# Optimization experiments

Measured on AMD Instinct MI355X. Metric: run time of the kernel, lower is better.

## Reference

```python
import jax, jax.numpy as jnp
import numpy as np

N_FILLERS = 10000
N_ROLES = 256
FILLER_DIM = 256
ROLE_DIM = 256
HIDDEN = 1024
B, S = 64, 128


def setup_inputs() -> dict:
    key = jax.random.key(0)
    k1, k2, k3, k4, k5, k6 = jax.random.split(key, 6)
    roles = jax.random.randint(k1, (B, S), 0, N_ROLES, dtype=jnp.int64 if jax.config.jax_enable_x64 else jnp.int32)
    hidden = jax.random.normal(k2, (1, B, HIDDEN), dtype=jnp.float32)
    filler_emb = jax.random.normal(k3, (N_FILLERS, FILLER_DIM), dtype=jnp.float32)
    role_emb = jax.random.normal(k4, (N_ROLES, ROLE_DIM), dtype=jnp.float32)
    role_emb = role_emb.at[0].set(0.0)  # padding_idx=0
    W = jax.random.normal(k5, (FILLER_DIM * ROLE_DIM, HIDDEN), dtype=jnp.float32) / np.sqrt(HIDDEN)
    b = jax.random.normal(k6, (FILLER_DIM * ROLE_DIM,), dtype=jnp.float32) * 0.01
    return {"roles": roles, "hidden": hidden, "filler_emb": filler_emb, "role_emb": role_emb, "W": W, "b": b}


def reference(roles, hidden, filler_emb, role_emb, W, b):
    fd = filler_emb.shape[1]
    rd = role_emb.shape[1]
    # input_layer: (1, B, hidden) -> (1, B, fd*rd)
    h = hidden @ W.T + b
    # transpose(0,1).transpose(1,2).view(-1, fd, rd): (B, fd, rd)
    h = jnp.transpose(h, (1, 2, 0)).reshape(-1, fd, rd)
    # role embedding with padding_idx=0 (row 0 is zero)
    role_table = role_emb.at[0].set(0.0)
    roles_e = role_table[roles]  # (B, S, rd)
    # bmm(roles_emb, hidden^T): (B, S, rd) x (B, rd, fd) -> (B, S, fd)
    fg = jnp.einsum('bsr,bfr->bsf', roles_e, h)
    # L2 distance to filler codebook via squared-norm trick: (B, S, n_fillers)
    d2 = (jnp.sum(fg * fg, axis=-1, keepdims=True)
          - 2.0 * jnp.einsum('bsf,nf->bsn', fg, filler_emb)
          + jnp.sum(filler_emb * filler_emb, axis=-1))
    dists = jnp.sqrt(jnp.maximum(d2, 0.0))
    log_probs = jax.nn.log_softmax(-dists, axis=-1)  # (B, S, n_fillers)
    preds = jnp.argmax(log_probs, axis=-1)  # top-1 indices, (B, S)
    return log_probs, preds
```

## Files before the change

### kernel.cpp

```cpp
#include <hip/hip_runtime.h>
#include <hip/hip_bf16.h>
#include <float.h>
#include <math.h>

#define ROWS 8192
#define NF   10000
#define NPAD 10240

typedef short s8v __attribute__((ext_vector_type(8)));
typedef float f4v __attribute__((ext_vector_type(4)));

#define GLD16(g, l) __builtin_amdgcn_global_load_lds((const __attribute__((address_space(1))) void*)(g), (__attribute__((address_space(3))) void*)(l), 16, 0, 0)

__device__ inline unsigned short f2bf(float x) {
  __hip_bfloat16 h = __float2bfloat16(x);
  return __builtin_bit_cast(unsigned short, h);
}
__device__ inline float bf2f(unsigned short u) {
  __hip_bfloat16 h = __builtin_bit_cast(__hip_bfloat16, u);
  return __bfloat162float(h);
}

__global__ __launch_bounds__(256) void k_cvt_filler(const float* __restrict__ filler,
                                                    unsigned short* __restrict__ fl2,
                                                    float* __restrict__ fln) {
  int row = blockIdx.x * 4 + (threadIdx.x >> 6);
  int lane = threadIdx.x & 63;
  if (row >= NPAD) return;
  if (row < NF) {
    float4 v = reinterpret_cast<const float4*>(filler + (size_t)row * 256)[lane];
    float s = v.x * v.x + v.y * v.y + v.z * v.z + v.w * v.w;
    #pragma unroll
    for (int off = 32; off >= 1; off >>= 1) s += __shfl_xor(s, off, 64);
    if (lane == 0) fln[row] = s;
    float xs[4] = {v.x, v.y, v.z, v.w};
    unsigned short h[4], lo[4];
    #pragma unroll
    for (int j = 0; j < 4; ++j) { h[j] = f2bf(xs[j]); lo[j] = f2bf(xs[j] - bf2f(h[j])); }
    uint2 hh = make_uint2(h[0] | ((unsigned)h[1] << 16), h[2] | ((unsigned)h[3] << 16));
    uint2 ll = make_uint2(lo[0] | ((unsigned)lo[1] << 16), lo[2] | ((unsigned)lo[3] << 16));
    *reinterpret_cast<uint2*>(fl2 + (size_t)row * 512 + lane * 4) = hh;
    *reinterpret_cast<uint2*>(fl2 + (size_t)row * 512 + 256 + lane * 4) = ll;
  } else {
    *reinterpret_cast<uint2*>(fl2 + (size_t)row * 512 + lane * 4) = make_uint2(0, 0);
    *reinterpret_cast<uint2*>(fl2 + (size_t)row * 512 + 256 + lane * 4) = make_uint2(0, 0);
    if (lane == 0) fln[row] = 1e30f;
  }
}

__global__ __launch_bounds__(256) void k_gemm1(const float* __restrict__ hidden,
                                               const float* __restrict__ W,
                                               const float* __restrict__ bias,
                                               float* __restrict__ ht) {
  __shared__ float As[64][68];
  __shared__ float Bs[64][136];
  __shared__ float biasS[128];
  const int tid = threadIdx.x;
  const int nbase = blockIdx.x * 128;
  const int r = nbase >> 8;
  const int f0 = nbase & 255;
  const int tm = tid >> 4, tn = tid & 15;
  const int m0 = tm * 4, n0 = tn * 8;

  if (tid < 128) biasS[tid] = bias[(size_t)(f0 + tid) * 256 + r];

  float acc[4][8];
  #pragma unroll
  for (int i = 0; i < 4; ++i)
    #pragma unroll
    for (int j = 0; j < 8; ++j) acc[i][j] = 0.f;

  for (int kt = 0; kt < 16; ++kt) {
    __syncthreads();
    #pragma unroll
    for (int i = 0; i < 4; ++i) {
      int q = tid + i * 256;
      int b = q >> 4, kq = q & 15;
      float4 v = *reinterpret_cast<const float4*>(hidden + (size_t)b * 1024 + kt * 64 + kq * 4);
      As[kq * 4 + 0][b] = v.x;
      As[kq * 4 + 1][b] = v.y;
      As[kq * 4 + 2][b] = v.z;
      As[kq * 4 + 3][b] = v.w;
    }
    #pragma unroll
    for (int i = 0; i < 8; ++i) {
      int q = tid + i * 256;
      int nl = q >> 4, kq = q & 15;
      size_t wrow = (size_t)(f0 + nl) * 256 + r;
      float4 v = *reinterpret_cast<const float4*>(W + wrow * 1024 + kt * 64 + kq * 4);
      Bs[kq * 4 + 0][nl] = v.x;
      Bs[kq * 4 + 1][nl] = v.y;
      Bs[kq * 4 + 2][nl] = v.z;
      Bs[kq * 4 + 3][nl] = v.w;
    }
    __syncthreads();
    #pragma unroll
    for (int kk = 0; kk < 64; ++kk) {
      float4 a  = *reinterpret_cast<const float4*>(&As[kk][m0]);
      float4 b0 = *reinterpret_cast<const float4*>(&Bs[kk][n0]);
      float4 b1 = *reinterpret_cast<const float4*>(&Bs[kk][n0 + 4]);
      float av[4] = {a.x, a.y, a.z, a.w};
      float bv[8] = {b0.x, b0.y, b0.z, b0.w, b1.x, b1.y, b1.z, b1.w};
      #pragma unroll
      for (int i = 0; i < 4; ++i)
        #pragma unroll
        for (int j = 0; j < 8; ++j) acc[i][j] += av[i] * bv[j];
    }
  }
  #pragma unroll
  for (int i = 0; i < 4; ++i) {
    int b = m0 + i;
    float4 o0 = make_float4(acc[i][0] + biasS[n0 + 0], acc[i][1] + biasS[n0 + 1],
                            acc[i][2] + biasS[n0 + 2], acc[i][3] + biasS[n0 + 3]);
    float4 o1 = make_float4(acc[i][4] + biasS[n0 + 4], acc[i][5] + biasS[n0 + 5],
                            acc[i][6] + biasS[n0 + 6], acc[i][7] + biasS[n0 + 7]);
    float* p = ht + (size_t)b * 65536 + nbase + n0;
    *reinterpret_cast<float4*>(p)     = o0;
    *reinterpret_cast<float4*>(p + 4) = o1;
  }
}

__global__ __launch_bounds__(256) void k_fg2(const int* __restrict__ roles,
                                             const float* __restrict__ role_emb,
                                             const float* __restrict__ ht,
                                             unsigned short* __restrict__ fg2,
                                             float* __restrict__ fgn) {
  __shared__ float As[64][40];
  __shared__ float Bs[64][264];
  __shared__ int sidx[32];
  const int tid = threadIdx.x;
  const int b = blockIdx.x >> 2;
  const int sbase = (blockIdx.x & 3) * 32;
  const int tm = tid >> 5, tn = tid & 31;
  const int m0 = tm * 4, n0 = tn * 8;
  if (tid < 32) sidx[tid] = roles[b * 128 + sbase + tid];

  float acc[4][8];
  #pragma unroll
  for (int i = 0; i < 4; ++i)
    #pragma unroll
    for (int j = 0; j < 8; ++j) acc[i][j] = 0.f;

  for (int kt = 0; kt < 4; ++kt) {
    __syncthreads();
    #pragma unroll
    for (int i = 0; i < 2; ++i) {
      int q = tid + i * 256;
      int s = q >> 4, rq = q & 15;
      float4 v = *reinterpret_cast<const float4*>(role_emb + (size_t)sidx[s] * 256 + kt * 64 + rq * 4);
      As[rq * 4 + 0][s] = v.x;
      As[rq * 4 + 1][s] = v.y;
      As[rq * 4 + 2][s] = v.z;
      As[rq * 4 + 3][s] = v.w;
    }
    #pragma unroll
    for (int i = 0; i < 16; ++i) {
      int q = tid + i * 256;
      int rr = q >> 6, fq = q & 63;
      float4 v = *reinterpret_cast<const float4*>(ht + (size_t)b * 65536 + (size_t)(kt * 64 + rr) * 256 + fq * 4);
      *reinterpret_cast<float4*>(&Bs[rr][fq * 4]) = v;
    }
    __syncthreads();
    #pragma unroll
    for (int kk = 0; kk < 64; ++kk) {
      float4 a  = *reinterpret_cast<const float4*>(&As[kk][m0]);
      float4 b0 = *reinterpret_cast<const float4*>(&Bs[kk][n0]);
      float4 b1 = *reinterpret_cast<const float4*>(&Bs[kk][n0 + 4]);
      float av[4] = {a.x, a.y, a.z, a.w};
      float bv[8] = {b0.x, b0.y, b0.z, b0.w, b1.x, b1.y, b1.z, b1.w};
      #pragma unroll
      for (int i = 0; i < 4; ++i)
        #pragma unroll
        for (int j = 0; j < 8; ++j) acc[i][j] += av[i] * bv[j];
    }
  }
  #pragma unroll
  for (int i = 0; i < 4; ++i) {
    const int grow = b * 128 + sbase + m0 + i;
    float nrm = 0.f;
    unsigned int hp[4], lp[4];
    #pragma unroll
    for (int j = 0; j < 8; j += 2) {
      float x0 = acc[i][j], x1 = acc[i][j + 1];
      nrm += x0 * x0 + x1 * x1;
      unsigned short h0 = f2bf(x0), h1 = f2bf(x1);
      unsigned short l0 = f2bf(x0 - bf2f(h0)), l1 = f2bf(x1 - bf2f(h1));
      hp[j >> 1] = h0 | ((unsigned)h1 << 16);
      lp[j >> 1] = l0 | ((unsigned)l1 << 16);
    }
    *reinterpret_cast<uint4*>(fg2 + (size_t)grow * 512 + n0)       = make_uint4(hp[0], hp[1], hp[2], hp[3]);
    *reinterpret_cast<uint4*>(fg2 + (size_t)grow * 512 + 256 + n0) = make_uint4(lp[0], lp[1], lp[2], lp[3]);
    #pragma unroll
    for (int msk = 1; msk <= 16; msk <<= 1) nrm += __shfl_xor(nrm, msk, 64);
    if (tn == 0) fgn[grow] = nrm;
  }
}

__global__ __launch_bounds__(512, 4) void k_dist(const unsigned short* __restrict__ fg2,
                                                 const unsigned short* __restrict__ fl2,
                                                 const float* __restrict__ fgn,
                                                 const float* __restrict__ fln,
                                                 float* __restrict__ out) {
  __shared__ __align__(16) char lds[2][32768];
  __shared__ float rn2s[128];
  const int tid = threadIdx.x;
  const int w = tid >> 6, l = tid & 63;
  const int g = l >> 4, lr = l & 15;
  const int mt  = (blockIdx.x & 7) * 8 + ((blockIdx.x >> 3) & 7);
  const int grp = blockIdx.x >> 6;
  const int rbase = mt << 7;
  const int wm = (w >> 2) << 6;
  const int wn = (w & 3) << 5;

  if (tid < 128) rn2s[tid] = fgn[rbase + tid];

  int rowC[2], swC[2];
  #pragma unroll
  for (int t = 0; t < 2; ++t) {
    int p = tid + t * 512;
    int row = p >> 3, c = p & 7;
    rowC[t] = row;
    swC[t] = (c ^ (row & 7)) << 3;
  }
  int offA[4], offB[2];
  #pragma unroll
  for (int i = 0; i < 4; ++i) { int r = wm + i * 16 + lr; offA[i] = r * 128 + ((g ^ (r & 7)) << 4); }
  #pragma unroll
  for (int j = 0; j < 2; ++j) { int r = wn + j * 16 + lr; offB[j] = 16384 + r * 128 + ((g ^ (r & 7)) << 4); }

  auto kAof = [](int kt) { return ((kt & 3) << 6) + ((kt >= 4 && kt < 8) ? 256 : 0); };
  auto kBof = [](int kt) { return ((kt & 3) << 6) + ((kt >= 8) ? 256 : 0); };

  auto stage = [&](int buf, int kt, int nb) {
    const int kA = kAof(kt), kB = kBof(kt);
    char* bA = &lds[buf][0]     + w * 1024;
    char* bB = &lds[buf][16384] + w * 1024;
    #pragma unroll
    for (int t = 0; t < 2; ++t) {
      GLD16(fg2 + ((size_t)(rbase + rowC[t]) * 512 + kA + swC[t]), bA + t * 8192);
      GLD16(fl2 + ((size_t)(nb    + rowC[t]) * 512 + kB + swC[t]), bB + t * 8192);
    }
  };

  stage(0, 0, grp << 7);
  __syncthreads();

  for (int s = 0; s < 10; ++s) {
    const int nt = grp + s * 8;
    const int nbase = nt << 7;
    float cnr[2];
    #pragma unroll
    for (int j = 0; j < 2; ++j) cnr[j] = fln[nbase + wn + j * 16 + lr];

    f4v acc[4][2];
    #pragma unroll
    for (int i = 0; i < 4; ++i)
      #pragma unroll
      for (int j = 0; j < 2; ++j) acc[i][j] = (f4v)0.f;

    for (int kt = 0; kt < 12; ++kt) {
      if (kt < 11)      stage((kt + 1) & 1, kt + 1, nbase);
      else if (s < 9)   stage(0, 0, (nt + 8) << 7);
      const char* A = lds[kt & 1];
      #pragma unroll
      for (int s2 = 0; s2 < 2; ++s2) {
        s8v va[4], vb[2];
        #pragma unroll
        for (int i = 0; i < 4; ++i) va[i] = *reinterpret_cast<const s8v*>(A + (offA[i] ^ (s2 << 6)));
        #pragma unroll
        for (int j = 0; j < 2; ++j) vb[j] = *reinterpret_cast<const s8v*>(A + (offB[j] ^ (s2 << 6)));
        #pragma unroll
        for (int i = 0; i < 4; ++i)
          #pragma unroll
          for (int j = 0; j < 2; ++j)
            acc[i][j] = __builtin_amdgcn_mfma_f32_16x16x32_bf16(va[i], vb[j], acc[i][j], 0, 0, 0);
      }
      __syncthreads();
    }

    float* scr = reinterpret_cast<float*>(&lds[1][0]);
    const int rem = NF - nbase;
    const int c4lim = (rem >= 128) ? 32 : (rem > 0 ? (rem >> 2) : 0);
    const int lbase = (wm >> 6) << 4;

    #pragma unroll
    for (int i = 0; i < 4; ++i) {
      #pragma unroll
      for (int j = 0; j < 2; ++j) {
        const int cloc = wn + (j << 4) + lr;
        #pragma unroll
        for (int r = 0; r < 4; ++r) {
          const int lrow = lbase + (g << 2) + r;
          const float r2 = rn2s[wm + (i << 4) + (g << 2) + r];
          float d = sqrtf(fmaxf(r2 - 2.0f * acc[i][j][r] + cnr[j], 0.f));
          scr[lrow * 132 + cloc] = d;
        }
      }
      __syncthreads();
      #pragma unroll
      for (int t2 = 0; t2 < 2; ++t2) {
        const int id2 = tid + (t2 << 9);
        const int rr2 = id2 >> 5, c4 = id2 & 31;
        f4v v = *reinterpret_cast<const f4v*>(scr + rr2 * 132 + (c4 << 2));
        if (c4 < c4lim) {
          const int grow = rbase + ((rr2 < 16) ? ((i << 4) + rr2) : (64 + (i << 4) + rr2 - 16));
          *reinterpret_cast<f4v*>(out + (size_t)grow * NF + nbase + (c4 << 2)) = v;
        }
      }
      __syncthreads();
    }
  }
}

__global__ __launch_bounds__(256) void k_final(float* __restrict__ out) {
  const int row = blockIdx.x;
  __shared__ __align__(16) float rowd[10000];
  __shared__ float red[16];
  const int t = threadIdx.x;
  const int w = t >> 6, l = t & 63;
  float* po = out + (size_t)row * NF;

  float bd = FLT_MAX; int bi = 0;
  for (int c = t; c < 2500; c += 256) {
    f4v v = __builtin_nontemporal_load(reinterpret_cast<const f4v*>(po) + c);
    *reinterpret_cast<f4v*>(&rowd[c * 4]) = v;
    const int base = c * 4;
    if (v[0] < bd) { bd = v[0]; bi = base; }
    if (v[1] < bd) { bd = v[1]; bi = base + 1; }
    if (v[2] < bd) { bd = v[2]; bi = base + 2; }
    if (v[3] < bd) { bd = v[3]; bi = base + 3; }
  }
  #pragma unroll
  for (int msk = 1; msk <= 32; msk <<= 1) {
    float od = __shfl_xor(bd, msk, 64);
    int   oi = __shfl_xor(bi, msk, 64);
    if (od < bd || (od == bd && oi < bi)) { bd = od; bi = oi; }
  }
  if (l == 0) { red[w * 2] = bd; red[w * 2 + 1] = (float)bi; }
  __syncthreads();
  if (t == 0) {
    float m = red[0], mi = red[1];
    #pragma unroll
    for (int c = 1; c < 4; ++c) {
      float od = red[c * 2], oi = red[c * 2 + 1];
      if (od < m || (od == m && oi < mi)) { m = od; mi = oi; }
    }
    red[8] = m; red[9] = mi;
  }
  __syncthreads();
  const float m = red[8];

  float s = 0.f;
  for (int c = t; c < 2500; c += 256) {
    f4v v = *reinterpret_cast<const f4v*>(&rowd[c * 4]);
    s += __expf(m - v[0]) + __expf(m - v[1]) + __expf(m - v[2]) + __expf(m - v[3]);
  }
  #pragma unroll
  for (int msk = 1; msk <= 32; msk <<= 1) s += __shfl_xor(s, msk, 64);
  if (l == 0) red[10 + w] = s;
  __syncthreads();
  if (t == 0) {
    float S = red[10] + red[11] + red[12] + red[13];
    red[14] = logf(S) - m;
    out[(size_t)ROWS * NF + row] = red[9];
  }
  __syncthreads();
  const float L = red[14];

  for (int c = t; c < 2500; c += 256) {
    f4v v = *reinterpret_cast<const f4v*>(&rowd[c * 4]);
    v = -v - L;
    __builtin_nontemporal_store(v, reinterpret_cast<f4v*>(po) + c);
  }
}

extern "C" void kernel_launch(void* const* d_in, const int* in_sizes, int n_in,
                              void* d_out, int out_size, void* d_ws, size_t ws_size,
                              hipStream_t stream) {
  const int*   roles   = (const int*)d_in[0];
  const float* hidden  = (const float*)d_in[1];
  const float* filler  = (const float*)d_in[2];
  const float* roleemb = (const float*)d_in[3];
  const float* W       = (const float*)d_in[4];
  const float* bias    = (const float*)d_in[5];
  float* out = (float*)d_out;

  float* ws = (float*)d_ws;
  float*          ht    = ws;
  unsigned short* fg2   = (unsigned short*)(ws + 4194304);
  unsigned short* fl2   = (unsigned short*)(ws + 6291456);
  float*          fgn   = ws + 8912896;
  float*          fln   = fgn + 8192;

  k_cvt_filler<<<2560, 256, 0, stream>>>(filler, fl2, fln);
  k_gemm1<<<512, 256, 0, stream>>>(hidden, W, bias, ht);
  k_fg2<<<256, 256, 0, stream>>>(roles, roleemb, ht, fg2, fgn);
  k_dist<<<512, 512, 0, stream>>>(fg2, fl2, fgn, fln, out);
  k_final<<<8192, 256, 0, stream>>>(out);
}
```

Baseline: 560.3 us.

## Halve k_dist LDS tile, double grid, write distances directly without LDS staging

```diff
diff --git a/kernel.cpp b/kernel.cpp
--- a/kernel.cpp
+++ b/kernel.cpp
@@ -196,17 +196,17 @@
   }
 }
 
-__global__ __launch_bounds__(512, 4) void k_dist(const unsigned short* __restrict__ fg2,
+__global__ __launch_bounds__(512, 8) void k_dist(const unsigned short* __restrict__ fg2,
                                                  const unsigned short* __restrict__ fl2,
                                                  const float* __restrict__ fgn,
                                                  const float* __restrict__ fln,
                                                  float* __restrict__ out) {
-  __shared__ __align__(16) char lds[2][32768];
+  __shared__ __align__(16) char lds[2][16384];
   __shared__ float rn2s[128];
   const int tid = threadIdx.x;
   const int w = tid >> 6, l = tid & 63;
   const int g = l >> 4, lr = l & 15;
-  const int mt  = (blockIdx.x & 7) * 8 + ((blockIdx.x >> 3) & 7);
+  const int mt  = ((blockIdx.x & 7) << 3) + ((blockIdx.x >> 3) & 7);
   const int grp = blockIdx.x >> 6;
   const int rbase = mt << 7;
   const int wm = (w >> 2) << 6;
@@ -214,39 +214,27 @@
 
   if (tid < 128) rn2s[tid] = fgn[rbase + tid];
 
-  int rowC[2], swC[2];
-  #pragma unroll
-  for (int t = 0; t < 2; ++t) {
-    int p = tid + t * 512;
-    int row = p >> 3, c = p & 7;
-    rowC[t] = row;
-    swC[t] = (c ^ (row & 7)) << 3;
-  }
+  const int rowC = tid >> 2, cC = tid & 3;
+  const int swC = (cC ^ ((rowC >> 1) & 3)) << 3;
   int offA[4], offB[2];
   #pragma unroll
-  for (int i = 0; i < 4; ++i) { int r = wm + i * 16 + lr; offA[i] = r * 128 + ((g ^ (r & 7)) << 4); }
-  #pragma unroll
-  for (int j = 0; j < 2; ++j) { int r = wn + j * 16 + lr; offB[j] = 16384 + r * 128 + ((g ^ (r & 7)) << 4); }
-
-  auto kAof = [](int kt) { return ((kt & 3) << 6) + ((kt >= 4 && kt < 8) ? 256 : 0); };
-  auto kBof = [](int kt) { return ((kt & 3) << 6) + ((kt >= 8) ? 256 : 0); };
+  for (int i = 0; i < 4; ++i) { int r = wm + i * 16 + lr; offA[i] = r * 64 + ((g ^ ((r >> 1) & 3)) << 4); }
+  #pragma unroll
+  for (int j = 0; j < 2; ++j) { int r = wn + j * 16 + lr; offB[j] = 8192 + r * 64 + ((g ^ ((r >> 1) & 3)) << 4); }
+
+  auto kAof = [](int kt) { return ((kt & 7) << 5) + ((kt >= 8 && kt < 16) ? 256 : 0); };
+  auto kBof = [](int kt) { return ((kt & 7) << 5) + ((kt >= 16) ? 256 : 0); };
 
   auto stage = [&](int buf, int kt, int nb) {
-    const int kA = kAof(kt), kB = kBof(kt);
-    char* bA = &lds[buf][0]     + w * 1024;
-    char* bB = &lds[buf][16384] + w * 1024;
-    #pragma unroll
-    for (int t = 0; t < 2; ++t) {
-      GLD16(fg2 + ((size_t)(rbase + rowC[t]) * 512 + kA + swC[t]), bA + t * 8192);
-      GLD16(fl2 + ((size_t)(nb    + rowC[t]) * 512 + kB + swC[t]), bB + t * 8192);
-    }
+    GLD16(fg2 + ((size_t)(rbase + rowC) * 512 + kAof(kt) + swC), &lds[buf][0]    + w * 1024);
+    GLD16(fl2 + ((size_t)(nb    + rowC) * 512 + kBof(kt) + swC), &lds[buf][8192] + w * 1024);
   };
 
   stage(0, 0, grp << 7);
   __syncthreads();
 
-  for (int s = 0; s < 10; ++s) {
-    const int nt = grp + s * 8;
+  for (int s = 0; s < 5; ++s) {
+    const int nt = grp + s * 16;
     const int nbase = nt << 7;
     float cnr[2];
     #pragma unroll
@@ -258,56 +246,37 @@
       #pragma unroll
       for (int j = 0; j < 2; ++j) acc[i][j] = (f4v)0.f;
 
-    for (int kt = 0; kt < 12; ++kt) {
-      if (kt < 11)      stage((kt + 1) & 1, kt + 1, nbase);
-      else if (s < 9)   stage(0, 0, (nt + 8) << 7);
+    for (int kt = 0; kt < 24; ++kt) {
+      if (kt < 23)    stage((kt + 1) & 1, kt + 1, nbase);
+      else if (s < 4) stage(0, 0, (nt + 16) << 7);
       const char* A = lds[kt & 1];
-      #pragma unroll
-      for (int s2 = 0; s2 < 2; ++s2) {
-        s8v va[4], vb[2];
+      s8v va[4], vb[2];
+      #pragma unroll
+      for (int i = 0; i < 4; ++i) va[i] = *reinterpret_cast<const s8v*>(A + offA[i]);
+      #pragma unroll
+      for (int j = 0; j < 2; ++j) vb[j] = *reinterpret_cast<const s8v*>(A + offB[j]);
+      #pragma unroll
+      for (int i = 0; i < 4; ++i)
         #pragma unroll
-        for (int i = 0; i < 4; ++i) va[i] = *reinterpret_cast<const s8v*>(A + (offA[i] ^ (s2 << 6)));
+        for (int j = 0; j < 2; ++j)
+          acc[i][j] = __builtin_amdgcn_mfma_f32_16x16x32_bf16(va[i], vb[j], acc[i][j], 0, 0, 0);
+      __syncthreads();
+    }
+
+    #pragma unroll
+    for (int i = 0; i < 4; ++i) {
+      #pragma unroll
+      for (int r = 0; r < 4; ++r) {
+        const int grow = rbase + wm + (i << 4) + (g << 2) + r;
+        const float r2 = rn2s[wm + (i << 4) + (g << 2) + r];
+        float* prow = out + (size_t)grow * NF + nbase;
         #pragma unroll
-        for (int j = 0; j < 2; ++j) vb[j] = *reinterpret_cast<const s8v*>(A + (offB[j] ^ (s2 << 6)));
-        #pragma unroll
-        for (int i = 0; i < 4; ++i)
-          #pragma unroll
-          for (int j = 0; j < 2; ++j)
-            acc[i][j] = __builtin_amdgcn_mfma_f32_16x16x32_bf16(va[i], vb[j], acc[i][j], 0, 0, 0);
-      }
-      __syncthreads();
-    }
-
-    float* scr = reinterpret_cast<float*>(&lds[1][0]);
-    const int rem = NF - nbase;
-    const int c4lim = (rem >= 128) ? 32 : (rem > 0 ? (rem >> 2) : 0);
-    const int lbase = (wm >> 6) << 4;
-
-    #pragma unroll
-    for (int i = 0; i < 4; ++i) {
-      #pragma unroll
-      for (int j = 0; j < 2; ++j) {
-        const int cloc = wn + (j << 4) + lr;
-        #pragma unroll
-        for (int r = 0; r < 4; ++r) {
-          const int lrow = lbase + (g << 2) + r;
-          const float r2 = rn2s[wm + (i << 4) + (g << 2) + r];
+        for (int j = 0; j < 2; ++j) {
+          const int cloc = wn + (j << 4) + lr;
           float d = sqrtf(fmaxf(r2 - 2.0f * acc[i][j][r] + cnr[j], 0.f));
-          scr[lrow * 132 + cloc] = d;
+          if (nbase + cloc < NF) prow[cloc] = d;
         }
       }
-      __syncthreads();
-      #pragma unroll
-      for (int t2 = 0; t2 < 2; ++t2) {
-        const int id2 = tid + (t2 << 9);
-        const int rr2 = id2 >> 5, c4 = id2 & 31;
-        f4v v = *reinterpret_cast<const f4v*>(scr + rr2 * 132 + (c4 << 2));
-        if (c4 < c4lim) {
-          const int grow = rbase + ((rr2 < 16) ? ((i << 4) + rr2) : (64 + (i << 4) + rr2 - 16));
-          *reinterpret_cast<f4v*>(out + (size_t)grow * NF + nbase + (c4 << 2)) = v;
-        }
-      }
-      __syncthreads();
     }
   }
 }
@@ -322,7 +291,7 @@
 
   float bd = FLT_MAX; int bi = 0;
   for (int c = t; c < 2500; c += 256) {
-    f4v v = __builtin_nontemporal_load(reinterpret_cast<const f4v*>(po) + c);
+    f4v v = *(reinterpret_cast<const f4v*>(po) + c);
     *reinterpret_cast<f4v*>(&rowd[c * 4]) = v;
     const int base = c * 4;
     if (v[0] < bd) { bd = v[0]; bi = base; }
@@ -395,6 +364,6 @@
   k_cvt_filler<<<2560, 256, 0, stream>>>(filler, fl2, fln);
   k_gemm1<<<512, 256, 0, stream>>>(hidden, W, bias, ht);
   k_fg2<<<256, 256, 0, stream>>>(roles, roleemb, ht, fg2, fgn);
-  k_dist<<<512, 512, 0, stream>>>(fg2, fl2, fgn, fln, out);
+  k_dist<<<1024, 512, 0, stream>>>(fg2, fl2, fgn, fln, out);
   k_final<<<8192, 256, 0, stream>>>(out);
 }
```

Result: slower. 628.6 us (+12.2%).

## Deepen GEMM prefetch pipeline with fine-grained waitcnt barriers and MFMA priority

Applied to the files above, without the earlier changes.

```diff
diff --git a/kernel.cpp b/kernel.cpp
--- a/kernel.cpp
+++ b/kernel.cpp
@@ -251,6 +251,7 @@
     float cnr[2];
     #pragma unroll
     for (int j = 0; j < 2; ++j) cnr[j] = fln[nbase + wn + j * 16 + lr];
+    stage(1, 1, nbase);
 
     f4v acc[4][2];
     #pragma unroll
@@ -259,23 +260,31 @@
       for (int j = 0; j < 2; ++j) acc[i][j] = (f4v)0.f;
 
     for (int kt = 0; kt < 12; ++kt) {
-      if (kt < 11)      stage((kt + 1) & 1, kt + 1, nbase);
-      else if (s < 9)   stage(0, 0, (nt + 8) << 7);
+      asm volatile("s_waitcnt vmcnt(4)" ::: "memory");
+      __builtin_amdgcn_s_barrier();
       const char* A = lds[kt & 1];
+      s8v va[2][4], vb[2][2];
       #pragma unroll
       for (int s2 = 0; s2 < 2; ++s2) {
-        s8v va[4], vb[2];
-        #pragma unroll
-        for (int i = 0; i < 4; ++i) va[i] = *reinterpret_cast<const s8v*>(A + (offA[i] ^ (s2 << 6)));
-        #pragma unroll
-        for (int j = 0; j < 2; ++j) vb[j] = *reinterpret_cast<const s8v*>(A + (offB[j] ^ (s2 << 6)));
+        #pragma unroll
+        for (int i = 0; i < 4; ++i) va[s2][i] = *reinterpret_cast<const s8v*>(A + (offA[i] ^ (s2 << 6)));
+        #pragma unroll
+        for (int j = 0; j < 2; ++j) vb[s2][j] = *reinterpret_cast<const s8v*>(A + (offB[j] ^ (s2 << 6)));
+      }
+      asm volatile("s_waitcnt lgkmcnt(0)" ::: "memory");
+      __builtin_amdgcn_sched_barrier(0);
+      __builtin_amdgcn_s_barrier();
+      if (kt < 10)       stage(kt & 1, kt + 2, nbase);
+      else if (kt == 10) stage(0, 0, (s < 9) ? ((nt + 8) << 7) : nbase);
+      __builtin_amdgcn_s_setprio(1);
+      #pragma unroll
+      for (int s2 = 0; s2 < 2; ++s2)
         #pragma unroll
         for (int i = 0; i < 4; ++i)
           #pragma unroll
           for (int j = 0; j < 2; ++j)
-            acc[i][j] = __builtin_amdgcn_mfma_f32_16x16x32_bf16(va[i], vb[j], acc[i][j], 0, 0, 0);
-      }
-      __syncthreads();
+            acc[i][j] = __builtin_amdgcn_mfma_f32_16x16x32_bf16(va[s2][i], vb[s2][j], acc[i][j], 0, 0, 0);
+      __builtin_amdgcn_s_setprio(0);
     }
 
     float* scr = reinterpret_cast<float*>(&lds[1][0]);
@@ -296,7 +305,8 @@
           scr[lrow * 132 + cloc] = d;
         }
       }
-      __syncthreads();
+      asm volatile("s_waitcnt lgkmcnt(0)" ::: "memory");
+      __builtin_amdgcn_s_barrier();
       #pragma unroll
       for (int t2 = 0; t2 < 2; ++t2) {
         const int id2 = tid + (t2 << 9);
@@ -307,8 +317,11 @@
           *reinterpret_cast<f4v*>(out + (size_t)grow * NF + nbase + (c4 << 2)) = v;
         }
       }
-      __syncthreads();
-    }
+      asm volatile("s_waitcnt lgkmcnt(0)" ::: "memory");
+      __builtin_amdgcn_s_barrier();
+    }
+    asm volatile("s_waitcnt vmcnt(0)" ::: "memory");
+    __builtin_amdgcn_s_barrier();
   }
 }
 
```

Result: slower. 628.3 us (+12.1%).

## Fuse per-tile min and exp-sum partials into distance kernel, simplify final pass

Applied to the files above, without the earlier changes.

```diff
diff --git a/kernel.cpp b/kernel.cpp
--- a/kernel.cpp
+++ b/kernel.cpp
@@ -200,14 +200,16 @@
                                                  const unsigned short* __restrict__ fl2,
                                                  const float* __restrict__ fgn,
                                                  const float* __restrict__ fln,
-                                                 float* __restrict__ out) {
+                                                 float* __restrict__ out,
+                                                 float* __restrict__ parts) {
   __shared__ __align__(16) char lds[2][32768];
   __shared__ float rn2s[128];
+  __shared__ float statS[128][12];
   const int tid = threadIdx.x;
   const int w = tid >> 6, l = tid & 63;
   const int g = l >> 4, lr = l & 15;
-  const int mt  = (blockIdx.x & 7) * 8 + ((blockIdx.x >> 3) & 7);
-  const int grp = blockIdx.x >> 6;
+  const int mt  = blockIdx.x >> 3;
+  const int grp = blockIdx.x & 7;
   const int rbase = mt << 7;
   const int wm = (w >> 2) << 6;
   const int wn = (w & 3) << 5;
@@ -286,14 +288,33 @@
     #pragma unroll
     for (int i = 0; i < 4; ++i) {
       #pragma unroll
-      for (int j = 0; j < 2; ++j) {
-        const int cloc = wn + (j << 4) + lr;
-        #pragma unroll
-        for (int r = 0; r < 4; ++r) {
-          const int lrow = lbase + (g << 2) + r;
-          const float r2 = rn2s[wm + (i << 4) + (g << 2) + r];
+      for (int r = 0; r < 4; ++r) {
+        const int lrow = lbase + (g << 2) + r;
+        const int rowloc = wm + (i << 4) + (g << 2) + r;
+        const float r2 = rn2s[rowloc];
+        float dv[2];
+        #pragma unroll
+        for (int j = 0; j < 2; ++j) {
+          const int cloc = wn + (j << 4) + lr;
           float d = sqrtf(fmaxf(r2 - 2.0f * acc[i][j][r] + cnr[j], 0.f));
+          dv[j] = d;
           scr[lrow * 132 + cloc] = d;
+        }
+        float bd; int bn;
+        if (dv[0] <= dv[1]) { bd = dv[0]; bn = nbase + wn + lr; }
+        else                { bd = dv[1]; bn = nbase + wn + 16 + lr; }
+        #pragma unroll
+        for (int msk = 1; msk <= 8; msk <<= 1) {
+          float od = __shfl_xor(bd, msk, 64);
+          int   on = __shfl_xor(bn, msk, 64);
+          if (od < bd || (od == bd && on < bn)) { bd = od; bn = on; }
+        }
+        float sE = __expf(bd - dv[0]) + __expf(bd - dv[1]);
+        #pragma unroll
+        for (int msk = 1; msk <= 8; msk <<= 1) sE += __shfl_xor(sE, msk, 64);
+        if (lr == 0) {
+          float* q = &statS[rowloc][(w & 3) * 3];
+          q[0] = bd; q[1] = sE; q[2] = (float)bn;
         }
       }
       __syncthreads();
@@ -304,71 +325,52 @@
         f4v v = *reinterpret_cast<const f4v*>(scr + rr2 * 132 + (c4 << 2));
         if (c4 < c4lim) {
           const int grow = rbase + ((rr2 < 16) ? ((i << 4) + rr2) : (64 + (i << 4) + rr2 - 16));
-          *reinterpret_cast<f4v*>(out + (size_t)grow * NF + nbase + (c4 << 2)) = v;
+          __builtin_nontemporal_store(v, reinterpret_cast<f4v*>(out + (size_t)grow * NF + nbase + (c4 << 2)));
         }
       }
       __syncthreads();
     }
-  }
-}
-
-__global__ __launch_bounds__(256) void k_final(float* __restrict__ out) {
+
+    if (tid < 128) {
+      const float* q = statS[tid];
+      float M = q[0], bn = q[2];
+      #pragma unroll
+      for (int c = 1; c < 4; ++c)
+        if (q[c * 3] < M) { M = q[c * 3]; bn = q[c * 3 + 2]; }
+      float S = 0.f;
+      #pragma unroll
+      for (int c = 0; c < 4; ++c) S += q[c * 3 + 1] * __expf(M - q[c * 3]);
+      f4v pv = {M, S, bn, 0.f};
+      reinterpret_cast<f4v*>(parts)[(size_t)(rbase + tid) * 80 + nt] = pv;
+    }
+    __syncthreads();
+  }
+}
+
+__global__ __launch_bounds__(256) void k_final(const float* __restrict__ parts,
+                                               float* __restrict__ out) {
   const int row = blockIdx.x;
-  __shared__ __align__(16) float rowd[10000];
-  __shared__ float red[16];
+  __shared__ __align__(16) f4v sm[80];
+  __shared__ float red[1];
   const int t = threadIdx.x;
-  const int w = t >> 6, l = t & 63;
   float* po = out + (size_t)row * NF;
 
-  float bd = FLT_MAX; int bi = 0;
+  if (t < 80) sm[t] = reinterpret_cast<const f4v*>(parts)[(size_t)row * 80 + t];
+  __syncthreads();
+  if (t == 0) {
+    float M = FLT_MAX, bn = 0.f;
+    for (int s = 0; s < 80; ++s)
+      if (sm[s][0] < M) { M = sm[s][0]; bn = sm[s][2]; }
+    float S = 0.f;
+    for (int s = 0; s < 80; ++s) S += sm[s][1] * __expf(M - sm[s][0]);
+    red[0] = logf(S) - M;
+    out[(size_t)ROWS * NF + row] = bn;
+  }
+  __syncthreads();
+  const float L = red[0];
+
   for (int c = t; c < 2500; c += 256) {
     f4v v = __builtin_nontemporal_load(reinterpret_cast<const f4v*>(po) + c);
-    *reinterpret_cast<f4v*>(&rowd[c * 4]) = v;
-    const int base = c * 4;
-    if (v[0] < bd) { bd = v[0]; bi = base; }
-    if (v[1] < bd) { bd = v[1]; bi = base + 1; }
-    if (v[2] < bd) { bd = v[2]; bi = base + 2; }
-    if (v[3] < bd) { bd = v[3]; bi = base + 3; }
-  }
-  #pragma unroll
-  for (int msk = 1; msk <= 32; msk <<= 1) {
-    float od = __shfl_xor(bd, msk, 64);
-    int   oi = __shfl_xor(bi, msk, 64);
-    if (od < bd || (od == bd && oi < bi)) { bd = od; bi = oi; }
-  }
-  if (l == 0) { red[w * 2] = bd; red[w * 2 + 1] = (float)bi; }
-  __syncthreads();
-  if (t == 0) {
-    float m = red[0], mi = red[1];
-    #pragma unroll
-    for (int c = 1; c < 4; ++c) {
-      float od = red[c * 2], oi = red[c * 2 + 1];
-      if (od < m || (od == m && oi < mi)) { m = od; mi = oi; }
-    }
-    red[8] = m; red[9] = mi;
-  }
-  __syncthreads();
-  const float m = red[8];
-
-  float s = 0.f;
-  for (int c = t; c < 2500; c += 256) {
-    f4v v = *reinterpret_cast<const f4v*>(&rowd[c * 4]);
-    s += __expf(m - v[0]) + __expf(m - v[1]) + __expf(m - v[2]) + __expf(m - v[3]);
-  }
-  #pragma unroll
-  for (int msk = 1; msk <= 32; msk <<= 1) s += __shfl_xor(s, msk, 64);
-  if (l == 0) red[10 + w] = s;
-  __syncthreads();
-  if (t == 0) {
-    float S = red[10] + red[11] + red[12] + red[13];
-    red[14] = logf(S) - m;
-    out[(size_t)ROWS * NF + row] = red[9];
-  }
-  __syncthreads();
-  const float L = red[14];
-
-  for (int c = t; c < 2500; c += 256) {
-    f4v v = *reinterpret_cast<const f4v*>(&rowd[c * 4]);
     v = -v - L;
     __builtin_nontemporal_store(v, reinterpret_cast<f4v*>(po) + c);
   }
@@ -391,10 +393,11 @@
   unsigned short* fl2   = (unsigned short*)(ws + 6291456);
   float*          fgn   = ws + 8912896;
   float*          fln   = fgn + 8192;
+  float*          parts = fln + 10240;
 
   k_cvt_filler<<<2560, 256, 0, stream>>>(filler, fl2, fln);
   k_gemm1<<<512, 256, 0, stream>>>(hidden, W, bias, ht);
   k_fg2<<<256, 256, 0, stream>>>(roles, roleemb, ht, fg2, fgn);
-  k_dist<<<512, 512, 0, stream>>>(fg2, fl2, fgn, fln, out);
-  k_final<<<8192, 256, 0, stream>>>(out);
-}
+  k_dist<<<512, 512, 0, stream>>>(fg2, fl2, fgn, fln, out, parts);
+  k_final<<<8192, 256, 0, stream>>>(parts, out);
+}
```

Result: slower. 825.5 us (+47.3%).
